# Performance work log

Hardware: AMD Instinct MI355X
Metric: run time of the kernel (lower is better)

Reference implementation:

```python
import jax, jax.numpy as jnp
import numpy as np

N = 12000      # nodes
E = 384000     # edges (avg degree 32)
IN, HID, OUT = 128, 128, 40
BETA, ITERS = 0.5, 25   # Bjorck order-2 projection params (module defaults)


def setup_inputs() -> dict:
    key = jax.random.key(0)
    ks = jax.random.split(key, 6)
    x = jax.random.normal(ks[0], (N, IN), jnp.float32)
    edge_index = jax.random.randint(ks[1], (2, E), 0, N, dtype=jnp.int32)
    W1 = jax.random.normal(ks[2], (HID, IN), jnp.float32)
    W2 = jax.random.normal(ks[3], (HID, HID), jnp.float32)
    lin_w = jax.random.normal(ks[4], (OUT, HID), jnp.float32) / np.float32(np.sqrt(HID))
    lin_b = jax.random.normal(ks[5], (OUT,), jnp.float32) * 0.01
    return {"x": x, "W1": W1, "W2": W2, "lin_w": lin_w, "lin_b": lin_b,
            "edge_index": edge_index}


def _bjorck(w):
    # order-2 Bjorck orthonormalization (beta fixed at 0.5):
    # w <- 15/8 w - 5/4 w(w^T w) + 3/8 w(w^T w)^2
    for _ in range(ITERS):
        wtw = w.T @ w
        w = 1.875 * w - 1.25 * (w @ wtw) + 0.375 * (w @ (wtw @ wtw))
    return w


def _orthonormal(W):
    # scale_values: sqrt(||W||_inf * ||W||_1) upper-bounds the spectral norm
    # (computed on .data in torch -> stop_gradient here)
    scaling = jnp.sqrt(jnp.abs(W).sum(axis=1).max() * jnp.abs(W).sum(axis=0).max())
    scaling = jax.lax.stop_gradient(scaling)
    return _bjorck(W.T / scaling).T  # [out, in]


def _normalized_adj(edge_index):
    # to_dense_adj (scatter-add) then D^{-1/2} A^T D^{-1/2} exactly as
    # normalize_tensor_adj: adj.dot(D^{-1/2}).T.dot(D^{-1/2})
    r, c = edge_index[0], edge_index[1]
    adj = jnp.zeros((N, N), jnp.float32).at[r, c].add(1.0)
    rowsum = adj.sum(axis=1)
    d = jnp.where(rowsum > 0, rowsum ** -0.5, 0.0)
    return d[:, None] * adj.T * d[None, :]


def reference(x, W1, W2, lin_w, lin_b, edge_index):
    norm_adj = _normalized_adj(edge_index)          # [N, N]
    h = jax.nn.relu(norm_adj @ (x @ _orthonormal(W1).T))   # [N, HID]
    h = jax.nn.relu(norm_adj @ (h @ _orthonormal(W2).T))   # [N, HID]
    # dropout inactive (eval mode)
    logits = h @ lin_w.T + lin_b                    # [N, OUT]
    return jax.nn.log_softmax(logits, axis=1)
```

## Files before the change

### kernel.cpp

```cpp
#include <hip/hip_runtime.h>
#include <math.h>

#define NN 12000
#define EE 384000
#define FF 128
#define NOUT 40
#define BJ_MAX 25
#define NWARM 8
#define EXIT_TOL 3e-3f
#define GEMM_BLOCKS ((NN + 63) / 64)

typedef __attribute__((ext_vector_type(8))) short bf16x8;
typedef __attribute__((ext_vector_type(4))) short s16x4;
typedef __attribute__((ext_vector_type(4))) float f32x4;
typedef unsigned short ushort_t;

__device__ __forceinline__ ushort_t f2bf(float x) {
  unsigned u = __float_as_uint(x);
  unsigned r = (u + 0x7FFFu + ((u >> 16) & 1u)) >> 16;
  return (ushort_t)r;
}
__device__ __forceinline__ float bf2f(ushort_t h) {
  return __uint_as_float(((unsigned)h) << 16);
}
__device__ __forceinline__ int swz(int r, int c) {
  return ((r << 8) + (c << 1)) ^ ((r & 7) << 4);
}

__global__ __launch_bounds__(1024) void scan_dinv_kernel(const int* __restrict__ cnt,
    int* __restrict__ rowstart, const float* __restrict__ degf, float* __restrict__ dinv) {
  __shared__ int sums[1024];
  int tid = threadIdx.x;
  const int CH = 12;
  int base = tid * CH;
  int local[CH];
  int s = 0;
  #pragma unroll
  for (int m = 0; m < CH; m++) {
    int idx = base + m;
    int v = (idx < NN) ? cnt[idx] : 0;
    local[m] = s;
    s += v;
  }
  sums[tid] = s;
  __syncthreads();
  for (int off = 1; off < 1024; off <<= 1) {
    int v = (tid >= off) ? sums[tid - off] : 0;
    __syncthreads();
    sums[tid] += v;
    __syncthreads();
  }
  int excl = (tid > 0) ? sums[tid - 1] : 0;
  #pragma unroll
  for (int m = 0; m < CH; m++) {
    int idx = base + m;
    if (idx < NN) rowstart[idx] = excl + local[m];
  }
  if (tid == 1023) rowstart[NN] = sums[1023];
  for (int i = tid; i < NN; i += 1024) {
    float dv = degf[i];
    dinv[i] = (dv > 0.0f) ? (1.0f / sqrtf(dv)) : 0.0f;
  }
}

__device__ __forceinline__ void mm_product(const char* Xh, const char* Xl,
    const char* Yh, const char* Yl, int R0, int C0, int lane, f32x4 (&acc)[2][4]) {
  int rl = lane & 15;
  int kq = (lane >> 4) * 8;
  #pragma unroll
  for (int k0 = 0; k0 < 128; k0 += 32) {
    bf16x8 ah[2], al[2];
    #pragma unroll
    for (int i = 0; i < 2; i++) {
      ah[i] = *(const bf16x8*)(Xh + swz(R0 + i * 16 + rl, k0 + kq));
      al[i] = *(const bf16x8*)(Xl + swz(R0 + i * 16 + rl, k0 + kq));
    }
    #pragma unroll
    for (int j = 0; j < 4; j++) {
      bf16x8 bh = *(const bf16x8*)(Yh + swz(C0 + j * 16 + rl, k0 + kq));
      bf16x8 bl = *(const bf16x8*)(Yl + swz(C0 + j * 16 + rl, k0 + kq));
      #pragma unroll
      for (int i = 0; i < 2; i++) {
        acc[i][j] = __builtin_amdgcn_mfma_f32_16x16x32_bf16(ah[i], bh, acc[i][j], 0, 0, 0);
        acc[i][j] = __builtin_amdgcn_mfma_f32_16x16x32_bf16(ah[i], bl, acc[i][j], 0, 0, 0);
        acc[i][j] = __builtin_amdgcn_mfma_f32_16x16x32_bf16(al[i], bh, acc[i][j], 0, 0, 0);
      }
    }
  }
}

__device__ __forceinline__ void store_C(char* Ch, char* Cl, int R0, int C0,
    int lane, f32x4 (&acc)[2][4]) {
  int cl = lane & 15, rq = (lane >> 4) * 4;
  #pragma unroll
  for (int i = 0; i < 2; i++)
  #pragma unroll
  for (int j = 0; j < 4; j++) {
    int col = C0 + j * 16 + cl;
    int row = R0 + i * 16 + rq;
    s16x4 hv, lv;
    #pragma unroll
    for (int t = 0; t < 4; t++) {
      float x = acc[i][j][t];
      ushort_t h = f2bf(x);
      ushort_t lo = f2bf(x - bf2f(h));
      hv[t] = (short)h; lv[t] = (short)lo;
    }
    *(s16x4*)(Ch + swz(col, row)) = hv;
    *(s16x4*)(Cl + swz(col, row)) = lv;
  }
}

__device__ __forceinline__ void store_CR(char* Ch, char* Cl, char* Rh, char* Rl,
    int R0, int C0, int lane, f32x4 (&acc)[2][4]) {
  int cl = lane & 15, rq = (lane >> 4) * 4;
  #pragma unroll
  for (int i = 0; i < 2; i++)
  #pragma unroll
  for (int j = 0; j < 4; j++) {
    int col = C0 + j * 16 + cl;
    int row = R0 + i * 16 + rq;
    s16x4 hv, lv;
    #pragma unroll
    for (int t = 0; t < 4; t++) {
      float x = acc[i][j][t];
      ushort_t h = f2bf(x);
      ushort_t lo = f2bf(x - bf2f(h));
      hv[t] = (short)h; lv[t] = (short)lo;
    }
    *(s16x4*)(Ch + swz(col, row)) = hv;
    *(s16x4*)(Cl + swz(col, row)) = lv;
    #pragma unroll
    for (int t = 0; t < 4; t++) {
      *(ushort_t*)(Rh + swz(row + t, col)) = (ushort_t)(unsigned short)hv[t];
      *(ushort_t*)(Rl + swz(row + t, col)) = (ushort_t)(unsigned short)lv[t];
    }
  }
}

__global__ __launch_bounds__(512) void bjorck_deg(const int* __restrict__ ei,
    float* __restrict__ degf, int* __restrict__ cnt,
    const float* __restrict__ W1, const float* __restrict__ W2,
    ushort_t* __restrict__ wfc) {
  if (blockIdx.x >= 2) {
    int e = (blockIdx.x - 2) * 512 + threadIdx.x;
    if (e < EE) {
      atomicAdd(&degf[ei[e]], 1.0f);
      atomicAdd(&cnt[ei[EE + e]], 1);
    }
    return;
  }

  __shared__ char lds[131072];
  __shared__ float wmax[8];
  char* P0h = lds;
  char* P0l = lds + 32768;
  char* P1h = lds + 65536;
  char* P1l = lds + 98304;
  const int L = blockIdx.x;
  const float* Wsrc = (L == 0) ? W1 : W2;
  int tid = threadIdx.x;
  int lane = tid & 63;
  int wv = tid >> 6;
  int R0 = (wv >> 1) * 32;
  int C0 = (wv & 1) * 64;

  float* f = (float*)lds;
  if (tid < 256) {
    float s = 0.0f;
    if (tid < 128) {
      for (int j = 0; j < FF; j++) s += fabsf(Wsrc[tid * FF + j]);
    } else {
      int c = tid - 128;
      for (int j = 0; j < FF; j++) s += fabsf(Wsrc[j * FF + c]);
    }
    f[tid] = s;
  }
  __syncthreads();
  if (tid == 0) {
    float rm = 0.0f, cm = 0.0f;
    for (int i = 0; i < 128; i++) { rm = fmaxf(rm, f[i]); cm = fmaxf(cm, f[128 + i]); }
    f[256] = 1.0f / sqrtf(rm * cm);
  }
  __syncthreads();
  float inv_s = f[256];
  __syncthreads();

  {
    int r = tid >> 2, c0 = (tid & 3) * 32;
    #pragma unroll
    for (int mm = 0; mm < 32; mm += 8) {
      bf16x8 hv, lv;
      #pragma unroll
      for (int t = 0; t < 8; t++) {
        float x = Wsrc[r * FF + c0 + mm + t] * inv_s;
        ushort_t h = f2bf(x);
        ushort_t lo = f2bf(x - bf2f(h));
        hv[t] = (short)h; lv[t] = (short)lo;
      }
      *(bf16x8*)(P0h + swz(r, c0 + mm)) = hv;
      *(bf16x8*)(P0l + swz(r, c0 + mm)) = lv;
      #pragma unroll
      for (int t = 0; t < 8; t++) {
        *(ushort_t*)(P1h + swz(c0 + mm + t, r)) = (ushort_t)(unsigned short)hv[t];
        *(ushort_t*)(P1l + swz(c0 + mm + t, r)) = (ushort_t)(unsigned short)lv[t];
      }
    }
  }
  __syncthreads();

  for (int it = 0; it < BJ_MAX; it++) {
    float ca, cb, cc;
    if (it < NWARM)       { ca = 3.4445f; cb = -4.7750f; cc = 2.0315f; }
    else if (it == NWARM) { ca = 2.1479f; cb = -1.7258f; cc = 0.5645f; }
    else                  { ca = 1.875f;  cb = -1.25f;   cc = 0.375f; }

    f32x4 m_acc[2][4] = {};
    mm_product(P0h, P0l, P0h, P0l, R0, C0, lane, m_acc);

    if (it > NWARM) {
      int cl = lane & 15, rq = (lane >> 4) * 4;
      float lmax = 0.0f;
      #pragma unroll
      for (int i = 0; i < 2; i++)
      #pragma unroll
      for (int j = 0; j < 4; j++)
      #pragma unroll
      for (int t = 0; t < 4; t++) {
        int row = R0 + i * 16 + rq + t;
        int col = C0 + j * 16 + cl;
        float d = m_acc[i][j][t] - ((row == col) ? 1.0f : 0.0f);
        lmax = fmaxf(lmax, fabsf(d));
      }
      #pragma unroll
      for (int off = 32; off; off >>= 1) lmax = fmaxf(lmax, __shfl_xor(lmax, off));
      if (lane == 0) wmax[wv] = lmax;
      __syncthreads();
      float gmax = 0.0f;
      #pragma unroll
      for (int w = 0; w < 8; w++) gmax = fmaxf(gmax, wmax[w]);
      if (gmax < EXIT_TOL) break;
    } else {
      __syncthreads();
    }
    store_C(P0h, P0l, R0, C0, lane, m_acc);
    __syncthreads();

    f32x4 p_acc[2][4] = {};
    mm_product(P0h, P0l, P0h, P0l, R0, C0, lane, p_acc);
    {
      int cl = lane & 15, rq = (lane >> 4) * 4;
      #pragma unroll
      for (int i = 0; i < 2; i++)
      #pragma unroll
      for (int j = 0; j < 4; j++)
      #pragma unroll
      for (int t = 0; t < 4; t++) {
        int row = R0 + i * 16 + rq + t;
        int col = C0 + j * 16 + cl;
        float pv = cb * m_acc[i][j][t] + cc * p_acc[i][j][t];
        if (row == col) pv += ca;
        p_acc[i][j][t] = pv;
      }
    }
    __syncthreads();
    store_C(P0h, P0l, R0, C0, lane, p_acc);
    __syncthreads();

    f32x4 v_acc[2][4] = {};
    mm_product(P0h, P0l, P1h, P1l, R0, C0, lane, v_acc);
    __syncthreads();
    store_CR(P1h, P1l, P0h, P0l, R0, C0, lane, v_acc);
    __syncthreads();
  }

  {
    ushort_t* oh = wfc + L * 32768;
    ushort_t* ol = oh + 16384;
    int r = tid >> 2;
    int q = tid & 3;
    #pragma unroll
    for (int b = 0; b < 4; b++) {
      int c0 = q * 32 + b * 8;
      bf16x8 hv = *(const bf16x8*)(P0h + swz(r, c0));
      bf16x8 lv = *(const bf16x8*)(P0l + swz(r, c0));
      *(bf16x8*)(oh + r * FF + c0) = hv;
      *(bf16x8*)(ol + r * FF + c0) = lv;
    }
  }
}

__global__ __launch_bounds__(256) void scatter_gemm1(const int* __restrict__ ei,
    const int* __restrict__ rowstart, int* __restrict__ fill, int* __restrict__ srcl,
    const float* __restrict__ X, const ushort_t* __restrict__ wc,
    float* __restrict__ Out) {
  if (blockIdx.x >= GEMM_BLOCKS) {
    int e = (blockIdx.x - GEMM_BLOCKS) * 256 + threadIdx.x;
    if (e < EE) {
      int r = ei[e], c = ei[EE + e];
      int pos = rowstart[c] + atomicAdd(&fill[c], 1);
      srcl[pos] = r;
    }
    return;
  }

  __shared__ char xlds[32768];
  char* Xh = xlds;
  char* Xl = xlds + 16384;
  int tid = threadIdx.x;
  int row0 = blockIdx.x * 64;

  {
    int r = tid >> 2;
    int q = (tid & 3) * 32;
    int gr = row0 + r;
    #pragma unroll
    for (int b = 0; b < 32; b += 8) {
      bf16x8 hv, lv;
      if (gr < NN) {
        const float4* xp4 = (const float4*)(X + gr * FF + q + b);
        float4 v0 = xp4[0];
        float4 v1 = xp4[1];
        float xv[8] = {v0.x, v0.y, v0.z, v0.w, v1.x, v1.y, v1.z, v1.w};
        #pragma unroll
        for (int t = 0; t < 8; t++) {
          ushort_t h = f2bf(xv[t]);
          hv[t] = (short)h;
          lv[t] = (short)f2bf(xv[t] - bf2f(h));
        }
      } else {
        #pragma unroll
        for (int t = 0; t < 8; t++) { hv[t] = 0; lv[t] = 0; }
      }
      *(bf16x8*)(Xh + swz(r, q + b)) = hv;
      *(bf16x8*)(Xl + swz(r, q + b)) = lv;
    }
  }
  __syncthreads();

  int lane = tid & 63, wv = tid >> 6;
  int R0 = (wv & 1) * 32;
  int C0 = (wv >> 1) * 64;
  int rl = lane & 15, kq = (lane >> 4) * 8;
  f32x4 acc[2][4] = {};
  #pragma unroll
  for (int k0 = 0; k0 < 128; k0 += 32) {
    bf16x8 ah[2], al[2];
    #pragma unroll
    for (int i = 0; i < 2; i++) {
      ah[i] = *(const bf16x8*)(Xh + swz(R0 + i * 16 + rl, k0 + kq));
      al[i] = *(const bf16x8*)(Xl + swz(R0 + i * 16 + rl, k0 + kq));
    }
    #pragma unroll
    for (int j = 0; j < 4; j++) {
      const ushort_t* bp = wc + (C0 + j * 16 + rl) * FF + k0 + kq;
      bf16x8 bh = *(const bf16x8*)bp;
      bf16x8 bl = *(const bf16x8*)(bp + 16384);
      #pragma unroll
      for (int i = 0; i < 2; i++) {
        acc[i][j] = __builtin_amdgcn_mfma_f32_16x16x32_bf16(ah[i], bh, acc[i][j], 0, 0, 0);
        acc[i][j] = __builtin_amdgcn_mfma_f32_16x16x32_bf16(ah[i], bl, acc[i][j], 0, 0, 0);
        acc[i][j] = __builtin_amdgcn_mfma_f32_16x16x32_bf16(al[i], bh, acc[i][j], 0, 0, 0);
      }
    }
  }
  int rq = (lane >> 4) * 4;
  #pragma unroll
  for (int i = 0; i < 2; i++)
  #pragma unroll
  for (int j = 0; j < 4; j++) {
    int col = C0 + j * 16 + rl;
    #pragma unroll
    for (int t = 0; t < 4; t++) {
      int node = row0 + R0 + i * 16 + rq + t;
      if (node < NN) Out[node * FF + col] = acc[i][j][t];
    }
  }
}

__global__ __launch_bounds__(256) void gemm_mfma(const float* __restrict__ X,
    const ushort_t* __restrict__ wc, float* __restrict__ Out) {
  __shared__ char xlds[32768];
  char* Xh = xlds;
  char* Xl = xlds + 16384;
  int tid = threadIdx.x;
  int row0 = blockIdx.x * 64;

  {
    int r = tid >> 2;
    int q = (tid & 3) * 32;
    int gr = row0 + r;
    #pragma unroll
    for (int b = 0; b < 32; b += 8) {
      bf16x8 hv, lv;
      if (gr < NN) {
        const float4* xp4 = (const float4*)(X + gr * FF + q + b);
        float4 v0 = xp4[0];
        float4 v1 = xp4[1];
        float xv[8] = {v0.x, v0.y, v0.z, v0.w, v1.x, v1.y, v1.z, v1.w};
        #pragma unroll
        for (int t = 0; t < 8; t++) {
          ushort_t h = f2bf(xv[t]);
          hv[t] = (short)h;
          lv[t] = (short)f2bf(xv[t] - bf2f(h));
        }
      } else {
        #pragma unroll
        for (int t = 0; t < 8; t++) { hv[t] = 0; lv[t] = 0; }
      }
      *(bf16x8*)(Xh + swz(r, q + b)) = hv;
      *(bf16x8*)(Xl + swz(r, q + b)) = lv;
    }
  }
  __syncthreads();

  int lane = tid & 63, wv = tid >> 6;
  int R0 = (wv & 1) * 32;
  int C0 = (wv >> 1) * 64;
  int rl = lane & 15, kq = (lane >> 4) * 8;
  f32x4 acc[2][4] = {};
  #pragma unroll
  for (int k0 = 0; k0 < 128; k0 += 32) {
    bf16x8 ah[2], al[2];
    #pragma unroll
    for (int i = 0; i < 2; i++) {
      ah[i] = *(const bf16x8*)(Xh + swz(R0 + i * 16 + rl, k0 + kq));
      al[i] = *(const bf16x8*)(Xl + swz(R0 + i * 16 + rl, k0 + kq));
    }
    #pragma unroll
    for (int j = 0; j < 4; j++) {
      const ushort_t* bp = wc + (C0 + j * 16 + rl) * FF + k0 + kq;
      bf16x8 bh = *(const bf16x8*)bp;
      bf16x8 bl = *(const bf16x8*)(bp + 16384);
      #pragma unroll
      for (int i = 0; i < 2; i++) {
        acc[i][j] = __builtin_amdgcn_mfma_f32_16x16x32_bf16(ah[i], bh, acc[i][j], 0, 0, 0);
        acc[i][j] = __builtin_amdgcn_mfma_f32_16x16x32_bf16(ah[i], bl, acc[i][j], 0, 0, 0);
        acc[i][j] = __builtin_amdgcn_mfma_f32_16x16x32_bf16(al[i], bh, acc[i][j], 0, 0, 0);
      }
    }
  }
  int rq = (lane >> 4) * 4;
  #pragma unroll
  for (int i = 0; i < 2; i++)
  #pragma unroll
  for (int j = 0; j < 4; j++) {
    int col = C0 + j * 16 + rl;
    #pragma unroll
    for (int t = 0; t < 4; t++) {
      int node = row0 + R0 + i * 16 + rq + t;
      if (node < NN) Out[node * FF + col] = acc[i][j][t];
    }
  }
}

__global__ __launch_bounds__(256) void spmm_relu(const float* __restrict__ G,
    float* __restrict__ Hout, const float* __restrict__ dinv,
    const int* __restrict__ rowstart, const int* __restrict__ srcl) {
  int g = threadIdx.x >> 5;
  int lane = threadIdx.x & 31;
  int row = blockIdx.x * 8 + g;
  int s = rowstart[row], e = rowstart[row + 1];
  const float4* G4 = (const float4*)G;
  float4 a0 = make_float4(0.f, 0.f, 0.f, 0.f);
  float4 a1 = make_float4(0.f, 0.f, 0.f, 0.f);
  int p = s;
  for (; p + 2 <= e; p += 2) {
    int r0 = srcl[p], r1 = srcl[p + 1];
    float d0 = dinv[r0], d1 = dinv[r1];
    float4 g0 = G4[r0 * 32 + lane];
    float4 g1 = G4[r1 * 32 + lane];
    a0.x += d0 * g0.x; a0.y += d0 * g0.y; a0.z += d0 * g0.z; a0.w += d0 * g0.w;
    a1.x += d1 * g1.x; a1.y += d1 * g1.y; a1.z += d1 * g1.z; a1.w += d1 * g1.w;
  }
  if (p < e) {
    int r0 = srcl[p];
    float d0 = dinv[r0];
    float4 g0 = G4[r0 * 32 + lane];
    a0.x += d0 * g0.x; a0.y += d0 * g0.y; a0.z += d0 * g0.z; a0.w += d0 * g0.w;
  }
  float dc = dinv[row];
  float4 o;
  o.x = fmaxf(dc * (a0.x + a1.x), 0.f); o.y = fmaxf(dc * (a0.y + a1.y), 0.f);
  o.z = fmaxf(dc * (a0.z + a1.z), 0.f); o.w = fmaxf(dc * (a0.w + a1.w), 0.f);
  ((float4*)Hout)[row * 32 + lane] = o;
}

__global__ __launch_bounds__(256) void spmm_head(const float* __restrict__ G,
    const float* __restrict__ dinv, const int* __restrict__ rowstart,
    const int* __restrict__ srcl, const float* __restrict__ lw,
    const float* __restrict__ lb, float* __restrict__ out) {
  __shared__ float slw[NOUT * 130];
  __shared__ float slb[64];
  __shared__ float sh[8][128];
  int tid = threadIdx.x;
  for (int i = tid; i < NOUT * 32; i += 256) {
    int r = i >> 5, c4 = i & 31;
    float4 v = ((const float4*)lw)[r * 32 + c4];
    float* dst = slw + r * 130 + c4 * 4;
    dst[0] = v.x; dst[1] = v.y; dst[2] = v.z; dst[3] = v.w;
  }
  if (tid < 64) slb[tid] = (tid < NOUT) ? lb[tid] : 0.0f;

  {
    int g = tid >> 5, lane32 = tid & 31;
    int row = blockIdx.x * 8 + g;
    int s = rowstart[row], e = rowstart[row + 1];
    const float4* G4 = (const float4*)G;
    float4 a0 = make_float4(0.f, 0.f, 0.f, 0.f);
    float4 a1 = make_float4(0.f, 0.f, 0.f, 0.f);
    int p = s;
    for (; p + 2 <= e; p += 2) {
      int r0 = srcl[p], r1 = srcl[p + 1];
      float d0 = dinv[r0], d1 = dinv[r1];
      float4 g0 = G4[r0 * 32 + lane32];
      float4 g1 = G4[r1 * 32 + lane32];
      a0.x += d0 * g0.x; a0.y += d0 * g0.y; a0.z += d0 * g0.z; a0.w += d0 * g0.w;
      a1.x += d1 * g1.x; a1.y += d1 * g1.y; a1.z += d1 * g1.z; a1.w += d1 * g1.w;
    }
    if (p < e) {
      int r0 = srcl[p];
      float d0 = dinv[r0];
      float4 g0 = G4[r0 * 32 + lane32];
      a0.x += d0 * g0.x; a0.y += d0 * g0.y; a0.z += d0 * g0.z; a0.w += d0 * g0.w;
    }
    float dc = dinv[row];
    float4 o;
    o.x = fmaxf(dc * (a0.x + a1.x), 0.f); o.y = fmaxf(dc * (a0.y + a1.y), 0.f);
    o.z = fmaxf(dc * (a0.z + a1.z), 0.f); o.w = fmaxf(dc * (a0.w + a1.w), 0.f);
    ((float4*)&sh[g][0])[lane32] = o;
  }
  __syncthreads();

  int lane = tid & 63, w = tid >> 6;
  int ll = (lane < NOUT) ? lane : 0;
  const float2* wrow = (const float2*)(slw + ll * 130);
  #pragma unroll
  for (int rr = 0; rr < 2; rr++) {
    int lrow = w * 2 + rr;
    int node = blockIdx.x * 8 + lrow;
    const float2* hrow = (const float2*)&sh[lrow][0];
    float val = slb[lane];
    #pragma unroll 4
    for (int k = 0; k < 64; k++) {
      float2 w2 = wrow[k];
      float2 h2 = hrow[k];
      val += w2.x * h2.x + w2.y * h2.y;
    }
    float m = (lane < NOUT) ? val : -INFINITY;
    for (int off = 32; off; off >>= 1) m = fmaxf(m, __shfl_down(m, off));
    m = __shfl(m, 0);
    float ex = (lane < NOUT) ? expf(val - m) : 0.0f;
    float ssum = ex;
    for (int off = 32; off; off >>= 1) ssum += __shfl_down(ssum, off);
    ssum = __shfl(ssum, 0);
    if (lane < NOUT) out[node * NOUT + lane] = val - m - logf(ssum);
  }
}

extern "C" void kernel_launch(void* const* d_in, const int* in_sizes, int n_in,
                              void* d_out, int out_size, void* d_ws, size_t ws_size,
                              hipStream_t stream) {
  const float* x  = (const float*)d_in[0];
  const float* W1 = (const float*)d_in[1];
  const float* W2 = (const float*)d_in[2];
  const float* lw = (const float*)d_in[3];
  const float* lb = (const float*)d_in[4];
  const int*   ei = (const int*)d_in[5];
  float* out = (float*)d_out;

  float* base = (float*)d_ws;
  float* wf   = base;
  float* degf = wf + 32768;
  int* cnt      = (int*)(degf + NN);
  int* fill     = cnt + NN;
  float* dinv = (float*)(fill + NN);
  int* rowstart = (int*)(dinv + NN);
  int* srcl     = rowstart + 12004;
  float* bufA = (float*)(srcl + EE);
  float* bufB = bufA + NN * FF;
  ushort_t* wfc = (ushort_t*)wf;

  (void)hipMemsetAsync(degf, 0, 3 * NN * sizeof(float), stream);

  bjorck_deg<<<2 + (EE + 511) / 512, 512, 0, stream>>>(ei, degf, cnt, W1, W2, wfc);
  scan_dinv_kernel<<<1, 1024, 0, stream>>>(cnt, rowstart, degf, dinv);
  scatter_gemm1<<<GEMM_BLOCKS + (EE + 255) / 256, 256, 0, stream>>>(
      ei, rowstart, fill, srcl, x, wfc, bufA);
  spmm_relu<<<NN / 8, 256, 0, stream>>>(bufA, bufB, dinv, rowstart, srcl);
  gemm_mfma<<<(NN + 63) / 64, 256, 0, stream>>>(bufB, wfc + 32768, bufA);
  spmm_head<<<NN / 8, 256, 0, stream>>>(bufA, dinv, rowstart, srcl, lw, lb, out);
}
```

Baseline: 235.0 us.

## Split Bjorck iterations across kernels to overlap with graph preprocessing and SpMM

The serial Bjorck orthonormalization, which runs on just two blocks, is split into four segments. Each segment's LDS state is saved to global memory and reloaded by the next, so the segments can run alongside degree counting, scan, CSR scatter and the first SpMM. The first layer is reordered to aggregate first (A·x) and then apply the GEMM with fused ReLU, since by then the W1 weights have finished converging. The cost is extra LDS state save/restore traffic and a second GEMM launch, and the serial Bjorck chain could still remain the critical path.

```diff
diff --git a/kernel.cpp b/kernel.cpp
--- a/kernel.cpp
+++ b/kernel.cpp
@@ -9,6 +9,9 @@
 #define NWARM 8
 #define EXIT_TOL 3e-3f
 #define GEMM_BLOCKS ((NN + 63) / 64)
+#define SEG1 3
+#define SEG2 6
+#define SEG3 9
 
 typedef __attribute__((ext_vector_type(8))) short bf16x8;
 typedef __attribute__((ext_vector_type(4))) short s16x4;
@@ -25,42 +28,6 @@
 }
 __device__ __forceinline__ int swz(int r, int c) {
   return ((r << 8) + (c << 1)) ^ ((r & 7) << 4);
-}
-
-__global__ __launch_bounds__(1024) void scan_dinv_kernel(const int* __restrict__ cnt,
-    int* __restrict__ rowstart, const float* __restrict__ degf, float* __restrict__ dinv) {
-  __shared__ int sums[1024];
-  int tid = threadIdx.x;
-  const int CH = 12;
-  int base = tid * CH;
-  int local[CH];
-  int s = 0;
-  #pragma unroll
-  for (int m = 0; m < CH; m++) {
-    int idx = base + m;
-    int v = (idx < NN) ? cnt[idx] : 0;
-    local[m] = s;
-    s += v;
-  }
-  sums[tid] = s;
-  __syncthreads();
-  for (int off = 1; off < 1024; off <<= 1) {
-    int v = (tid >= off) ? sums[tid - off] : 0;
-    __syncthreads();
-    sums[tid] += v;
-    __syncthreads();
-  }
-  int excl = (tid > 0) ? sums[tid - 1] : 0;
-  #pragma unroll
-  for (int m = 0; m < CH; m++) {
-    int idx = base + m;
-    if (idx < NN) rowstart[idx] = excl + local[m];
-  }
-  if (tid == 1023) rowstart[NN] = sums[1023];
-  for (int i = tid; i < NN; i += 1024) {
-    float dv = degf[i];
-    dinv[i] = (dv > 0.0f) ? (1.0f / sqrtf(dv)) : 0.0f;
-  }
 }
 
 __device__ __forceinline__ void mm_product(const char* Xh, const char* Xl,
@@ -138,55 +105,44 @@
   }
 }
 
-__global__ __launch_bounds__(512) void bjorck_deg(const int* __restrict__ ei,
-    float* __restrict__ degf, int* __restrict__ cnt,
+__device__ void bjorck_segment(int L, int s_it, int e_it, int is_last,
     const float* __restrict__ W1, const float* __restrict__ W2,
-    ushort_t* __restrict__ wfc) {
-  if (blockIdx.x >= 2) {
-    int e = (blockIdx.x - 2) * 512 + threadIdx.x;
-    if (e < EE) {
-      atomicAdd(&degf[ei[e]], 1.0f);
-      atomicAdd(&cnt[ei[EE + e]], 1);
-    }
-    return;
-  }
-
+    ushort_t* __restrict__ wfc, char* __restrict__ state) {
   __shared__ char lds[131072];
   __shared__ float wmax[8];
   char* P0h = lds;
   char* P0l = lds + 32768;
   char* P1h = lds + 65536;
   char* P1l = lds + 98304;
-  const int L = blockIdx.x;
   const float* Wsrc = (L == 0) ? W1 : W2;
   int tid = threadIdx.x;
   int lane = tid & 63;
   int wv = tid >> 6;
   int R0 = (wv >> 1) * 32;
   int C0 = (wv & 1) * 64;
-
-  float* f = (float*)lds;
-  if (tid < 256) {
-    float s = 0.0f;
-    if (tid < 128) {
-      for (int j = 0; j < FF; j++) s += fabsf(Wsrc[tid * FF + j]);
-    } else {
-      int c = tid - 128;
-      for (int j = 0; j < FF; j++) s += fabsf(Wsrc[j * FF + c]);
-    }
-    f[tid] = s;
-  }
-  __syncthreads();
-  if (tid == 0) {
-    float rm = 0.0f, cm = 0.0f;
-    for (int i = 0; i < 128; i++) { rm = fmaxf(rm, f[i]); cm = fmaxf(cm, f[128 + i]); }
-    f[256] = 1.0f / sqrtf(rm * cm);
-  }
-  __syncthreads();
-  float inv_s = f[256];
-  __syncthreads();
-
-  {
+  char* st = state + L * 131072;
+
+  if (s_it == 0) {
+    float* f = (float*)lds;
+    if (tid < 256) {
+      float s = 0.0f;
+      if (tid < 128) {
+        for (int j = 0; j < FF; j++) s += fabsf(Wsrc[tid * FF + j]);
+      } else {
+        int c = tid - 128;
+        for (int j = 0; j < FF; j++) s += fabsf(Wsrc[j * FF + c]);
+      }
+      f[tid] = s;
+    }
+    __syncthreads();
+    if (tid == 0) {
+      float rm = 0.0f, cm = 0.0f;
+      for (int i = 0; i < 128; i++) { rm = fmaxf(rm, f[i]); cm = fmaxf(cm, f[128 + i]); }
+      f[256] = 1.0f / sqrtf(rm * cm);
+    }
+    __syncthreads();
+    float inv_s = f[256];
+    __syncthreads();
     int r = tid >> 2, c0 = (tid & 3) * 32;
     #pragma unroll
     for (int mm = 0; mm < 32; mm += 8) {
@@ -206,10 +162,16 @@
         *(ushort_t*)(P1l + swz(c0 + mm + t, r)) = (ushort_t)(unsigned short)lv[t];
       }
     }
-  }
-  __syncthreads();
-
-  for (int it = 0; it < BJ_MAX; it++) {
+    __syncthreads();
+  } else {
+    int4* dst = (int4*)lds;
+    const int4* src = (const int4*)st;
+    for (int i = tid; i < 8192; i += 512) dst[i] = src[i];
+    __syncthreads();
+  }
+
+  int done = 0;
+  for (int it = s_it; it < e_it; it++) {
     float ca, cb, cc;
     if (it < NWARM)       { ca = 3.4445f; cb = -4.7750f; cc = 2.0315f; }
     else if (it == NWARM) { ca = 2.1479f; cb = -1.7258f; cc = 0.5645f; }
@@ -239,7 +201,7 @@
       float gmax = 0.0f;
       #pragma unroll
       for (int w = 0; w < 8; w++) gmax = fmaxf(gmax, wmax[w]);
-      if (gmax < EXIT_TOL) break;
+      if (gmax < EXIT_TOL) { done = 1; break; }
     } else {
       __syncthreads();
     }
@@ -274,7 +236,7 @@
     __syncthreads();
   }
 
-  {
+  if (done || is_last) {
     ushort_t* oh = wfc + L * 32768;
     ushort_t* ol = oh + 16384;
     int r = tid >> 2;
@@ -287,15 +249,78 @@
       *(bf16x8*)(oh + r * FF + c0) = hv;
       *(bf16x8*)(ol + r * FF + c0) = lv;
     }
-  }
-}
-
-__global__ __launch_bounds__(256) void scatter_gemm1(const int* __restrict__ ei,
+  } else {
+    const int4* src = (const int4*)lds;
+    int4* dst = (int4*)st;
+    for (int i = tid; i < 8192; i += 512) dst[i] = src[i];
+  }
+}
+
+__device__ void scan512(const int* __restrict__ cnt, int* __restrict__ rowstart,
+    const float* __restrict__ degf, float* __restrict__ dinv) {
+  __shared__ int sums[512];
+  int tid = threadIdx.x;
+  const int CH = 24;
+  int base = tid * CH;
+  int local[CH];
+  int s = 0;
+  #pragma unroll
+  for (int m = 0; m < CH; m++) {
+    int idx = base + m;
+    int v = (idx < NN) ? cnt[idx] : 0;
+    local[m] = s;
+    s += v;
+  }
+  sums[tid] = s;
+  __syncthreads();
+  for (int off = 1; off < 512; off <<= 1) {
+    int v = (tid >= off) ? sums[tid - off] : 0;
+    __syncthreads();
+    sums[tid] += v;
+    __syncthreads();
+  }
+  int excl = (tid > 0) ? sums[tid - 1] : 0;
+  #pragma unroll
+  for (int m = 0; m < CH; m++) {
+    int idx = base + m;
+    if (idx < NN) rowstart[idx] = excl + local[m];
+  }
+  if (tid == 511) rowstart[NN] = sums[511];
+  for (int i = tid; i < NN; i += 512) {
+    float dv = degf[i];
+    dinv[i] = (dv > 0.0f) ? (1.0f / sqrtf(dv)) : 0.0f;
+  }
+}
+
+__global__ __launch_bounds__(512) void k1_seg_deg(const int* __restrict__ ei,
+    float* __restrict__ degf, int* __restrict__ cnt,
+    const float* __restrict__ W1, const float* __restrict__ W2,
+    ushort_t* __restrict__ wfc, char* __restrict__ state) {
+  if (blockIdx.x >= 2) {
+    int e = (blockIdx.x - 2) * 512 + threadIdx.x;
+    if (e < EE) {
+      atomicAdd(&degf[ei[e]], 1.0f);
+      atomicAdd(&cnt[ei[EE + e]], 1);
+    }
+    return;
+  }
+  bjorck_segment(blockIdx.x, 0, SEG1, 0, W1, W2, wfc, state);
+}
+
+__global__ __launch_bounds__(512) void k2_seg_scan(const int* __restrict__ cnt,
+    int* __restrict__ rowstart, const float* __restrict__ degf, float* __restrict__ dinv,
+    const float* __restrict__ W1, const float* __restrict__ W2,
+    ushort_t* __restrict__ wfc, char* __restrict__ state) {
+  if (blockIdx.x == 2) { scan512(cnt, rowstart, degf, dinv); return; }
+  bjorck_segment(blockIdx.x, SEG1, SEG2, 0, W1, W2, wfc, state);
+}
+
+__global__ __launch_bounds__(512) void k3_seg_scatter(const int* __restrict__ ei,
     const int* __restrict__ rowstart, int* __restrict__ fill, int* __restrict__ srcl,
-    const float* __restrict__ X, const ushort_t* __restrict__ wc,
-    float* __restrict__ Out) {
-  if (blockIdx.x >= GEMM_BLOCKS) {
-    int e = (blockIdx.x - GEMM_BLOCKS) * 256 + threadIdx.x;
+    const float* __restrict__ W1, const float* __restrict__ W2,
+    ushort_t* __restrict__ wfc, char* __restrict__ state) {
+  if (blockIdx.x >= 2) {
+    int e = (blockIdx.x - 2) * 512 + threadIdx.x;
     if (e < EE) {
       int r = ei[e], c = ei[EE + e];
       int pos = rowstart[c] + atomicAdd(&fill[c], 1);
@@ -303,7 +328,48 @@
     }
     return;
   }
-
+  bjorck_segment(blockIdx.x, SEG2, SEG3, 0, W1, W2, wfc, state);
+}
+
+__global__ __launch_bounds__(512) void k4_seg_spmm(const float* __restrict__ X,
+    float* __restrict__ Sout, const float* __restrict__ dinv,
+    const int* __restrict__ rowstart, const int* __restrict__ srcl,
+    const float* __restrict__ W1, const float* __restrict__ W2,
+    ushort_t* __restrict__ wfc, char* __restrict__ state) {
+  if (blockIdx.x >= 2) {
+    int g = threadIdx.x >> 5, lane32 = threadIdx.x & 31;
+    int row = (blockIdx.x - 2) * 16 + g;
+    int s = rowstart[row], e = rowstart[row + 1];
+    const float4* G4 = (const float4*)X;
+    float4 a0 = make_float4(0.f, 0.f, 0.f, 0.f);
+    float4 a1 = make_float4(0.f, 0.f, 0.f, 0.f);
+    int p = s;
+    for (; p + 2 <= e; p += 2) {
+      int r0 = srcl[p], r1 = srcl[p + 1];
+      float d0 = dinv[r0], d1 = dinv[r1];
+      float4 g0 = G4[r0 * 32 + lane32];
+      float4 g1 = G4[r1 * 32 + lane32];
+      a0.x += d0 * g0.x; a0.y += d0 * g0.y; a0.z += d0 * g0.z; a0.w += d0 * g0.w;
+      a1.x += d1 * g1.x; a1.y += d1 * g1.y; a1.z += d1 * g1.z; a1.w += d1 * g1.w;
+    }
+    if (p < e) {
+      int r0 = srcl[p];
+      float d0 = dinv[r0];
+      float4 g0 = G4[r0 * 32 + lane32];
+      a0.x += d0 * g0.x; a0.y += d0 * g0.y; a0.z += d0 * g0.z; a0.w += d0 * g0.w;
+    }
+    float dc = dinv[row];
+    float4 o;
+    o.x = dc * (a0.x + a1.x); o.y = dc * (a0.y + a1.y);
+    o.z = dc * (a0.z + a1.z); o.w = dc * (a0.w + a1.w);
+    ((float4*)Sout)[row * 32 + lane32] = o;
+    return;
+  }
+  bjorck_segment(blockIdx.x, SEG3, BJ_MAX, 1, W1, W2, wfc, state);
+}
+
+__global__ __launch_bounds__(256) void gemm_mfma(const float* __restrict__ X,
+    const ushort_t* __restrict__ wc, float* __restrict__ Out, int do_relu) {
   __shared__ char xlds[32768];
   char* Xh = xlds;
   char* Xl = xlds + 16384;
@@ -373,117 +439,11 @@
     #pragma unroll
     for (int t = 0; t < 4; t++) {
       int node = row0 + R0 + i * 16 + rq + t;
-      if (node < NN) Out[node * FF + col] = acc[i][j][t];
-    }
-  }
-}
-
-__global__ __launch_bounds__(256) void gemm_mfma(const float* __restrict__ X,
-    const ushort_t* __restrict__ wc, float* __restrict__ Out) {
-  __shared__ char xlds[32768];
-  char* Xh = xlds;
-  char* Xl = xlds + 16384;
-  int tid = threadIdx.x;
-  int row0 = blockIdx.x * 64;
-
-  {
-    int r = tid >> 2;
-    int q = (tid & 3) * 32;
-    int gr = row0 + r;
-    #pragma unroll
-    for (int b = 0; b < 32; b += 8) {
-      bf16x8 hv, lv;
-      if (gr < NN) {
-        const float4* xp4 = (const float4*)(X + gr * FF + q + b);
-        float4 v0 = xp4[0];
-        float4 v1 = xp4[1];
-        float xv[8] = {v0.x, v0.y, v0.z, v0.w, v1.x, v1.y, v1.z, v1.w};
-        #pragma unroll
-        for (int t = 0; t < 8; t++) {
-          ushort_t h = f2bf(xv[t]);
-          hv[t] = (short)h;
-          lv[t] = (short)f2bf(xv[t] - bf2f(h));
-        }
-      } else {
-        #pragma unroll
-        for (int t = 0; t < 8; t++) { hv[t] = 0; lv[t] = 0; }
-      }
-      *(bf16x8*)(Xh + swz(r, q + b)) = hv;
-      *(bf16x8*)(Xl + swz(r, q + b)) = lv;
-    }
-  }
-  __syncthreads();
-
-  int lane = tid & 63, wv = tid >> 6;
-  int R0 = (wv & 1) * 32;
-  int C0 = (wv >> 1) * 64;
-  int rl = lane & 15, kq = (lane >> 4) * 8;
-  f32x4 acc[2][4] = {};
-  #pragma unroll
-  for (int k0 = 0; k0 < 128; k0 += 32) {
-    bf16x8 ah[2], al[2];
-    #pragma unroll
-    for (int i = 0; i < 2; i++) {
-      ah[i] = *(const bf16x8*)(Xh + swz(R0 + i * 16 + rl, k0 + kq));
-      al[i] = *(const bf16x8*)(Xl + swz(R0 + i * 16 + rl, k0 + kq));
-    }
-    #pragma unroll
-    for (int j = 0; j < 4; j++) {
-      const ushort_t* bp = wc + (C0 + j * 16 + rl) * FF + k0 + kq;
-      bf16x8 bh = *(const bf16x8*)bp;
-      bf16x8 bl = *(const bf16x8*)(bp + 16384);
-      #pragma unroll
-      for (int i = 0; i < 2; i++) {
-        acc[i][j] = __builtin_amdgcn_mfma_f32_16x16x32_bf16(ah[i], bh, acc[i][j], 0, 0, 0);
-        acc[i][j] = __builtin_amdgcn_mfma_f32_16x16x32_bf16(ah[i], bl, acc[i][j], 0, 0, 0);
-        acc[i][j] = __builtin_amdgcn_mfma_f32_16x16x32_bf16(al[i], bh, acc[i][j], 0, 0, 0);
-      }
-    }
-  }
-  int rq = (lane >> 4) * 4;
-  #pragma unroll
-  for (int i = 0; i < 2; i++)
-  #pragma unroll
-  for (int j = 0; j < 4; j++) {
-    int col = C0 + j * 16 + rl;
-    #pragma unroll
-    for (int t = 0; t < 4; t++) {
-      int node = row0 + R0 + i * 16 + rq + t;
-      if (node < NN) Out[node * FF + col] = acc[i][j][t];
-    }
-  }
-}
-
-__global__ __launch_bounds__(256) void spmm_relu(const float* __restrict__ G,
-    float* __restrict__ Hout, const float* __restrict__ dinv,
-    const int* __restrict__ rowstart, const int* __restrict__ srcl) {
-  int g = threadIdx.x >> 5;
-  int lane = threadIdx.x & 31;
-  int row = blockIdx.x * 8 + g;
-  int s = rowstart[row], e = rowstart[row + 1];
-  const float4* G4 = (const float4*)G;
-  float4 a0 = make_float4(0.f, 0.f, 0.f, 0.f);
-  float4 a1 = make_float4(0.f, 0.f, 0.f, 0.f);
-  int p = s;
-  for (; p + 2 <= e; p += 2) {
-    int r0 = srcl[p], r1 = srcl[p + 1];
-    float d0 = dinv[r0], d1 = dinv[r1];
-    float4 g0 = G4[r0 * 32 + lane];
-    float4 g1 = G4[r1 * 32 + lane];
-    a0.x += d0 * g0.x; a0.y += d0 * g0.y; a0.z += d0 * g0.z; a0.w += d0 * g0.w;
-    a1.x += d1 * g1.x; a1.y += d1 * g1.y; a1.z += d1 * g1.z; a1.w += d1 * g1.w;
-  }
-  if (p < e) {
-    int r0 = srcl[p];
-    float d0 = dinv[r0];
-    float4 g0 = G4[r0 * 32 + lane];
-    a0.x += d0 * g0.x; a0.y += d0 * g0.y; a0.z += d0 * g0.z; a0.w += d0 * g0.w;
-  }
-  float dc = dinv[row];
-  float4 o;
-  o.x = fmaxf(dc * (a0.x + a1.x), 0.f); o.y = fmaxf(dc * (a0.y + a1.y), 0.f);
-  o.z = fmaxf(dc * (a0.z + a1.z), 0.f); o.w = fmaxf(dc * (a0.w + a1.w), 0.f);
-  ((float4*)Hout)[row * 32 + lane] = o;
+      float v = acc[i][j][t];
+      if (do_relu) v = fmaxf(v, 0.0f);
+      if (node < NN) Out[node * FF + col] = v;
+    }
+  }
 }
 
 __global__ __launch_bounds__(256) void spmm_head(const float* __restrict__ G,
@@ -579,15 +539,17 @@
   int* srcl     = rowstart + 12004;
   float* bufA = (float*)(srcl + EE);
   float* bufB = bufA + NN * FF;
+  char* state = (char*)(bufB + NN * FF);
   ushort_t* wfc = (ushort_t*)wf;
 
   (void)hipMemsetAsync(degf, 0, 3 * NN * sizeof(float), stream);
 
-  bjorck_deg<<<2 + (EE + 511) / 512, 512, 0, stream>>>(ei, degf, cnt, W1, W2, wfc);
-  scan_dinv_kernel<<<1, 1024, 0, stream>>>(cnt, rowstart, degf, dinv);
-  scatter_gemm1<<<GEMM_BLOCKS + (EE + 255) / 256, 256, 0, stream>>>(
-      ei, rowstart, fill, srcl, x, wfc, bufA);
-  spmm_relu<<<NN / 8, 256, 0, stream>>>(bufA, bufB, dinv, rowstart, srcl);
-  gemm_mfma<<<(NN + 63) / 64, 256, 0, stream>>>(bufB, wfc + 32768, bufA);
+  k1_seg_deg<<<2 + (EE + 511) / 512, 512, 0, stream>>>(ei, degf, cnt, W1, W2, wfc, state);
+  k2_seg_scan<<<3, 512, 0, stream>>>(cnt, rowstart, degf, dinv, W1, W2, wfc, state);
+  k3_seg_scatter<<<2 + (EE + 511) / 512, 512, 0, stream>>>(ei, rowstart, fill, srcl, W1, W2, wfc, state);
+  k4_seg_spmm<<<2 + NN / 16, 512, 0, stream>>>(x, bufA, dinv, rowstart, srcl, W1, W2, wfc, state);
+
+  gemm_mfma<<<GEMM_BLOCKS, 256, 0, stream>>>(bufA, wfc, bufB, 1);
+  gemm_mfma<<<GEMM_BLOCKS, 256, 0, stream>>>(bufB, wfc + 32768, bufA, 0);
   spmm_head<<<NN / 8, 256, 0, stream>>>(bufA, dinv, rowstart, srcl, lw, lb, out);
 }
```

Result: slower. 241.3 us (+2.7%).
